# Kernel optimization log

Measured on AMD Instinct MI355X. Metric: run time of the kernel, lower is better.

Reference implementation:

```python
import jax, jax.numpy as jnp
import numpy as np

E = 8          # num_experts
K = 2          # num_experts_per_tok
NORM_TOPK = True
B, S, D, F = 2, 1024, 2048, 1024  # batch, seq, hidden, moe_intermediate


def _kaiming_uniform(key, shape):
    # moe_fused_kaiming_uniform_: bound = sqrt(3*5 / in_features), in_features = shape[-1]
    bound = float(np.sqrt(3.0 * 5.0 / shape[-1]))
    return jax.random.uniform(key, shape, jnp.float32, -bound, bound)


def setup_inputs() -> dict:
    key = jax.random.key(0)
    k0, k1, k2, k3, k4 = jax.random.split(key, 5)
    gate_bound = float(1.0 / np.sqrt(D))  # nn.Linear default init
    return {
        "hidden_states": jax.random.normal(k0, (B, S, D), jnp.float32),
        "gate_w": jax.random.uniform(k1, (E, D), jnp.float32, -gate_bound, gate_bound),
        "w_gate_proj": _kaiming_uniform(k2, (E, F, D)),
        "w_up_proj": _kaiming_uniform(k3, (E, F, D)),
        "w_down_proj": _kaiming_uniform(k4, (E, D, F)),
    }


def reference(hidden_states, gate_w, w_gate_proj, w_up_proj, w_down_proj):
    b, s, d = hidden_states.shape
    x = hidden_states.reshape(-1, d)                      # [T, D]
    T = x.shape[0]

    # Router: softmax in fp32, top-k, optional renorm
    router_logits = x @ gate_w.T                          # [T, E]
    probs = jax.nn.softmax(router_logits.astype(jnp.float32), axis=-1)
    routing_weights, selected = jax.lax.top_k(probs, K)   # [T, K], [T, K]
    if NORM_TOPK:
        routing_weights = routing_weights / routing_weights.sum(-1, keepdims=True)
    routing_weights = routing_weights.astype(x.dtype)

    # Dense combine weights: c[t, e] = sum_k rw[t,k] * (sel[t,k]==e)
    combine = jnp.zeros((T, E), x.dtype).at[jnp.arange(T)[:, None], selected].add(routing_weights)

    # Expert SwiGLU FFN (dense over experts; combine zeros out unrouted experts,
    # identical math to sorted grouped-GEMM dispatch in the original)
    g = jnp.einsum('td,efd->tef', x, w_gate_proj)         # [T, E, F]
    u = jnp.einsum('td,efd->tef', x, w_up_proj)           # [T, E, F]
    h = jax.nn.silu(g) * u                                # [T, E, F]
    out = jnp.einsum('tef,edf,te->td', h, w_down_proj, combine)  # [T, D]

    return out.reshape(b, s, d), router_logits
```

## Files before the change

kernel.cpp:

```cpp
#include <hip/hip_runtime.h>
#include <stdint.h>

#define T_TOK 2048
#define DIM   2048
#define FDIM  1024
#define NE    8
#define MAXTILES 40

typedef __attribute__((ext_vector_type(8))) short short8;
typedef __attribute__((ext_vector_type(4))) float f32x4;

__device__ __forceinline__ unsigned short f2b(float f) {
  union { float f; unsigned int i; } x; x.f = f;
  unsigned int r = x.i + 0x7fffu + ((x.i >> 16) & 1u);
  return (unsigned short)(r >> 16);
}

__device__ __forceinline__ void async16(void* lds, const void* g) {
  __builtin_amdgcn_global_load_lds(
      (const __attribute__((address_space(1))) void*)g,
      (__attribute__((address_space(3))) void*)lds, 16, 0, 0);
}

__global__ __launch_bounds__(256) void cvt_w_k(const float* __restrict__ src,
                                               unsigned short* __restrict__ dst)
{
  size_t i = ((size_t)blockIdx.x * 256 + threadIdx.x) * 8;
  float4 a = *(const float4*)(src + i);
  float4 b = *(const float4*)(src + i + 4);
  ushort4 o0, o1;
  o0.x = f2b(a.x); o0.y = f2b(a.y); o0.z = f2b(a.z); o0.w = f2b(a.w);
  o1.x = f2b(b.x); o1.y = f2b(b.y); o1.z = f2b(b.z); o1.w = f2b(b.w);
  *(ushort4*)(dst + i) = o0;
  *(ushort4*)(dst + i + 4) = o1;
}

__global__ __launch_bounds__(256) void router_k(
    const float* __restrict__ x, const float* __restrict__ gw,
    float* __restrict__ topkw, int* __restrict__ topke, int* __restrict__ counts,
    float* __restrict__ logits_out, unsigned short* __restrict__ xb)
{
  int wave = threadIdx.x >> 6, lane = threadIdx.x & 63;
  int t = blockIdx.x * 4 + wave;
  const float* xr = x + (size_t)t * DIM;
  unsigned short* xbr = xb + (size_t)t * DIM;
  float acc[NE];
#pragma unroll
  for (int e = 0; e < NE; e++) acc[e] = 0.f;
  for (int d = lane * 4; d < DIM; d += 256) {
    float4 xv = *(const float4*)(xr + d);
    ushort4 xo;
    xo.x = f2b(xv.x); xo.y = f2b(xv.y); xo.z = f2b(xv.z); xo.w = f2b(xv.w);
    *(ushort4*)(xbr + d) = xo;
#pragma unroll
    for (int e = 0; e < NE; e++) {
      float4 gv = *(const float4*)(gw + e * DIM + d);
      acc[e] += xv.x * gv.x + xv.y * gv.y + xv.z * gv.z + xv.w * gv.w;
    }
  }
#pragma unroll
  for (int off = 32; off > 0; off >>= 1) {
#pragma unroll
    for (int e = 0; e < NE; e++) acc[e] += __shfl_down(acc[e], off);
  }
  if (lane == 0) {
    float m = acc[0];
#pragma unroll
    for (int e = 1; e < NE; e++) m = fmaxf(m, acc[e]);
    float p[NE];
#pragma unroll
    for (int e = 0; e < NE; e++) p[e] = __expf(acc[e] - m);
    int e0 = 0;
#pragma unroll
    for (int e = 1; e < NE; e++) if (acc[e] > acc[e0]) e0 = e;
    int e1 = -1;
#pragma unroll
    for (int e = 0; e < NE; e++) if (e != e0 && (e1 < 0 || acc[e] > acc[e1])) e1 = e;
    float s = p[e0] + p[e1];
    topkw[t * 2] = p[e0] / s;
    topkw[t * 2 + 1] = p[e1] / s;
    topke[t * 2] = e0; topke[t * 2 + 1] = e1;
    atomicAdd(&counts[e0], 1);
    atomicAdd(&counts[e1], 1);
#pragma unroll
    for (int e = 0; e < NE; e++) logits_out[t * NE + e] = acc[e];
  }
}

__global__ void scan_k(const int* __restrict__ counts, int* __restrict__ offsets,
                       int* __restrict__ cursors, int4* __restrict__ tiles,
                       int* __restrict__ ntiles)
{
  if (threadIdx.x == 0 && blockIdx.x == 0) {
    int o = 0, nt = 0;
    for (int e = 0; e < NE; e++) {
      offsets[e] = o; cursors[e] = o;
      int c = counts[e];
      for (int r = 0; r < c; r += 128) {
        int rows = c - r < 128 ? c - r : 128;
        tiles[nt] = make_int4(e, o + r, rows, 0);
        nt++;
      }
      o += c;
    }
    offsets[NE] = o;
    *ntiles = nt;
  }
}

__global__ void scatter_k(const int* __restrict__ topke, int* __restrict__ cursors,
                          int* __restrict__ perm)
{
  int i = blockIdx.x * blockDim.x + threadIdx.x;
  int e = topke[i];
  int s = atomicAdd(&cursors[e], 1);
  perm[s] = i;
}


__global__ __launch_bounds__(256) void gemm1_bf_k(
    const unsigned short* __restrict__ xb,
    const unsigned short* __restrict__ wgb,
    const unsigned short* __restrict__ wub,
    const int* __restrict__ perm, const float* __restrict__ topkw,
    const int4* __restrict__ tiles, const int* __restrict__ ntiles,
    unsigned short* __restrict__ H)
{
  __shared__ short As[128 * 32];
  __shared__ short Bgs[64 * 32];
  __shared__ short Bus[64 * 32];
  __shared__ int rowtok[128];
  __shared__ float roww[128];

  if (blockIdx.x >= *ntiles) return;
  int4 tm = tiles[blockIdx.x];
  int e = tm.x, row0 = tm.y, nrows = tm.z;
  int tid = threadIdx.x;
  if (tid < 128) {
    int r = tid < nrows ? tid : (nrows - 1);
    int pid = perm[row0 + r];
    rowtok[tid] = pid >> 1;
    roww[tid] = topkw[pid];
  }
  __syncthreads();

  int f0 = blockIdx.y * 64;
  int crow = tid >> 2;
  int ccol = (tid & 3) * 8;
  const unsigned short* a0 = xb + (size_t)rowtok[crow] * DIM + ccol;
  const unsigned short* a1 = xb + (size_t)rowtok[crow + 64] * DIM + ccol;
  const unsigned short* bg = wgb + ((size_t)e * FDIM + f0 + crow) * DIM + ccol;
  const unsigned short* bu = wub + ((size_t)e * FDIM + f0 + crow) * DIM + ccol;
  short* as0 = As + tid * 8;
  short* as1 = As + (256 + tid) * 8;
  short* bgs = Bgs + tid * 8;
  short* bus = Bus + tid * 8;

  int wave = tid >> 6, lane = tid & 63;
  int wm = wave >> 1, wn = wave & 1;
  int lrow = lane & 15, quad = lane >> 4;

  f32x4 accg[4][2], accu[4][2];
#pragma unroll
  for (int i = 0; i < 4; i++)
#pragma unroll
    for (int j = 0; j < 2; j++) {
      accg[i][j] = (f32x4){0.f, 0.f, 0.f, 0.f};
      accu[i][j] = (f32x4){0.f, 0.f, 0.f, 0.f};
    }

  const short* arp = As + (wm * 64 + lrow) * 32 + quad * 8;
  const short* bgp = Bgs + (wn * 32 + lrow) * 32 + quad * 8;
  const short* bup = Bus + (wn * 32 + lrow) * 32 + quad * 8;

#pragma unroll 1
  for (int k0 = 0; k0 < DIM; k0 += 32) {
    async16(as0, a0 + k0);
    async16(as1, a1 + k0);
    async16(bgs, bg + k0);
    async16(bus, bu + k0);
    __syncthreads();
    short8 af[4], bgf[2], buf2[2];
#pragma unroll
    for (int i = 0; i < 4; i++) af[i] = *(const short8*)(arp + i * 16 * 32);
#pragma unroll
    for (int j = 0; j < 2; j++) {
      bgf[j]  = *(const short8*)(bgp + j * 16 * 32);
      buf2[j] = *(const short8*)(bup + j * 16 * 32);
    }
#pragma unroll
    for (int i = 0; i < 4; i++)
#pragma unroll
      for (int j = 0; j < 2; j++) {
        accg[i][j] = __builtin_amdgcn_mfma_f32_16x16x32_bf16(af[i], bgf[j], accg[i][j], 0, 0, 0);
        accu[i][j] = __builtin_amdgcn_mfma_f32_16x16x32_bf16(af[i], buf2[j], accu[i][j], 0, 0, 0);
      }
    __syncthreads();
  }

#pragma unroll
  for (int i = 0; i < 4; i++) {
#pragma unroll
    for (int reg = 0; reg < 4; reg++) {
      int r = wm * 64 + i * 16 + quad * 4 + reg;
      if (r < nrows) {
        float w = roww[r];
#pragma unroll
        for (int j = 0; j < 2; j++) {
          float g = accg[i][j][reg], u = accu[i][j][reg];
          float h = g * u * w / (1.f + __expf(-g));
          H[(size_t)(row0 + r) * FDIM + f0 + wn * 32 + j * 16 + lrow] = f2b(h);
        }
      }
    }
  }
}

__global__ __launch_bounds__(256) void gemm2_bf_k(
    const unsigned short* __restrict__ H,
    const unsigned short* __restrict__ wdb,
    const int* __restrict__ perm,
    const int4* __restrict__ tiles, const int* __restrict__ ntiles,
    float* __restrict__ out)
{
  __shared__ short Hs[128 * 32];
  __shared__ short Bs[128 * 32];
  __shared__ int rowtok[128];

  if (blockIdx.x >= *ntiles) return;
  int4 tm = tiles[blockIdx.x];
  int e = tm.x, row0 = tm.y, nrows = tm.z;
  int tid = threadIdx.x;
  if (tid < 128) {
    int r = tid < nrows ? tid : (nrows - 1);
    rowtok[tid] = perm[row0 + r] >> 1;
  }
  __syncthreads();

  int d0 = blockIdx.y * 128;
  int crow = tid >> 2, ccol = (tid & 3) * 8;
  const unsigned short* a0 = H + (size_t)(row0 + crow) * FDIM + ccol;
  const unsigned short* a1 = H + (size_t)(row0 + crow + 64) * FDIM + ccol;
  const unsigned short* b0 = wdb + ((size_t)e * DIM + d0 + crow) * FDIM + ccol;
  const unsigned short* b1 = b0 + (size_t)64 * FDIM;
  short* hs0 = Hs + tid * 8;
  short* hs1 = Hs + (256 + tid) * 8;
  short* bs0 = Bs + tid * 8;
  short* bs1 = Bs + (256 + tid) * 8;

  int wave = tid >> 6, lane = tid & 63;
  int wm = wave >> 1, wn = wave & 1;
  int lrow = lane & 15, quad = lane >> 4;

  f32x4 acc[4][4];
#pragma unroll
  for (int i = 0; i < 4; i++)
#pragma unroll
    for (int j = 0; j < 4; j++) acc[i][j] = (f32x4){0.f, 0.f, 0.f, 0.f};

  const short* arp = Hs + (wm * 64 + lrow) * 32 + quad * 8;
  const short* brp = Bs + (wn * 64 + lrow) * 32 + quad * 8;

#pragma unroll 1
  for (int k0 = 0; k0 < FDIM; k0 += 32) {
    async16(hs0, a0 + k0);
    async16(hs1, a1 + k0);
    async16(bs0, b0 + k0);
    async16(bs1, b1 + k0);
    __syncthreads();
    short8 af[4], bf[4];
#pragma unroll
    for (int i = 0; i < 4; i++) af[i] = *(const short8*)(arp + i * 16 * 32);
#pragma unroll
    for (int j = 0; j < 4; j++) bf[j] = *(const short8*)(brp + j * 16 * 32);
#pragma unroll
    for (int i = 0; i < 4; i++)
#pragma unroll
      for (int j = 0; j < 4; j++)
        acc[i][j] = __builtin_amdgcn_mfma_f32_16x16x32_bf16(af[i], bf[j], acc[i][j], 0, 0, 0);
    __syncthreads();
  }

#pragma unroll
  for (int i = 0; i < 4; i++) {
#pragma unroll
    for (int reg = 0; reg < 4; reg++) {
      int r = wm * 64 + i * 16 + quad * 4 + reg;
      if (r < nrows) {
        int t = rowtok[r];
#pragma unroll
        for (int j = 0; j < 4; j++) {
          atomicAdd(&out[(size_t)t * DIM + d0 + wn * 64 + j * 16 + lrow], acc[i][j][reg]);
        }
      }
    }
  }
}


__global__ __launch_bounds__(256) void gemm1_f32_k(
    const unsigned short* __restrict__ xb,
    const float* __restrict__ wg,
    const float* __restrict__ wu,
    const int* __restrict__ perm, const float* __restrict__ topkw,
    const int4* __restrict__ tiles, const int* __restrict__ ntiles,
    unsigned short* __restrict__ H)
{
  __shared__ short As[128 * 32];
  __shared__ short Bgs[64 * 32];
  __shared__ short Bus[64 * 32];
  __shared__ int rowtok[128];
  __shared__ float roww[128];

  if (blockIdx.x >= *ntiles) return;
  int4 tm = tiles[blockIdx.x];
  int e = tm.x, row0 = tm.y, nrows = tm.z;
  int tid = threadIdx.x;
  if (tid < 128) {
    int r = tid < nrows ? tid : (nrows - 1);
    int pid = perm[row0 + r];
    rowtok[tid] = pid >> 1;
    roww[tid] = topkw[pid];
  }
  __syncthreads();

  int f0 = blockIdx.y * 64;
  int crow = tid >> 2;
  int ccol = (tid & 3) * 8;
  const unsigned short* a0 = xb + (size_t)rowtok[crow] * DIM + ccol;
  const unsigned short* a1 = xb + (size_t)rowtok[crow + 64] * DIM + ccol;
  const float* bg32 = wg + ((size_t)e * FDIM + f0 + crow) * DIM + ccol;
  const float* bu32 = wu + ((size_t)e * FDIM + f0 + crow) * DIM + ccol;
  short* as0 = As + tid * 8;
  short* as1 = As + (256 + tid) * 8;

  int wave = tid >> 6, lane = tid & 63;
  int wm = wave >> 1, wn = wave & 1;
  int lrow = lane & 15, quad = lane >> 4;

  f32x4 accg[4][2], accu[4][2];
#pragma unroll
  for (int i = 0; i < 4; i++)
#pragma unroll
    for (int j = 0; j < 2; j++) {
      accg[i][j] = (f32x4){0.f, 0.f, 0.f, 0.f};
      accu[i][j] = (f32x4){0.f, 0.f, 0.f, 0.f};
    }

  const short* arp = As + (wm * 64 + lrow) * 32 + quad * 8;
  const short* bgp = Bgs + (wn * 32 + lrow) * 32 + quad * 8;
  const short* bup = Bus + (wn * 32 + lrow) * 32 + quad * 8;

#pragma unroll 1
  for (int k0 = 0; k0 < DIM; k0 += 32) {
    async16(as0, a0 + k0);
    async16(as1, a1 + k0);
    float4 g0 = *(const float4*)(bg32 + k0);
    float4 g1 = *(const float4*)(bg32 + k0 + 4);
    float4 u0 = *(const float4*)(bu32 + k0);
    float4 u1 = *(const float4*)(bu32 + k0 + 4);
    short8 gs, us;
    gs[0] = f2b(g0.x); gs[1] = f2b(g0.y); gs[2] = f2b(g0.z); gs[3] = f2b(g0.w);
    gs[4] = f2b(g1.x); gs[5] = f2b(g1.y); gs[6] = f2b(g1.z); gs[7] = f2b(g1.w);
    us[0] = f2b(u0.x); us[1] = f2b(u0.y); us[2] = f2b(u0.z); us[3] = f2b(u0.w);
    us[4] = f2b(u1.x); us[5] = f2b(u1.y); us[6] = f2b(u1.z); us[7] = f2b(u1.w);
    *(short8*)(Bgs + tid * 8) = gs;
    *(short8*)(Bus + tid * 8) = us;
    __syncthreads();
    short8 af[4], bgf[2], buf2[2];
#pragma unroll
    for (int i = 0; i < 4; i++) af[i] = *(const short8*)(arp + i * 16 * 32);
#pragma unroll
    for (int j = 0; j < 2; j++) {
      bgf[j]  = *(const short8*)(bgp + j * 16 * 32);
      buf2[j] = *(const short8*)(bup + j * 16 * 32);
    }
#pragma unroll
    for (int i = 0; i < 4; i++)
#pragma unroll
      for (int j = 0; j < 2; j++) {
        accg[i][j] = __builtin_amdgcn_mfma_f32_16x16x32_bf16(af[i], bgf[j], accg[i][j], 0, 0, 0);
        accu[i][j] = __builtin_amdgcn_mfma_f32_16x16x32_bf16(af[i], buf2[j], accu[i][j], 0, 0, 0);
      }
    __syncthreads();
  }

#pragma unroll
  for (int i = 0; i < 4; i++) {
#pragma unroll
    for (int reg = 0; reg < 4; reg++) {
      int r = wm * 64 + i * 16 + quad * 4 + reg;
      if (r < nrows) {
        float w = roww[r];
#pragma unroll
        for (int j = 0; j < 2; j++) {
          float g = accg[i][j][reg], u = accu[i][j][reg];
          float h = g * u * w / (1.f + __expf(-g));
          H[(size_t)(row0 + r) * FDIM + f0 + wn * 32 + j * 16 + lrow] = f2b(h);
        }
      }
    }
  }
}

__global__ __launch_bounds__(256) void gemm2_f32_k(
    const unsigned short* __restrict__ H,
    const float* __restrict__ wd,
    const int* __restrict__ perm,
    const int4* __restrict__ tiles, const int* __restrict__ ntiles,
    float* __restrict__ out)
{
  __shared__ short Hs[128 * 32];
  __shared__ short Bs[64 * 32];
  __shared__ int rowtok[128];

  if (blockIdx.x >= *ntiles) return;
  int4 tm = tiles[blockIdx.x];
  int e = tm.x, row0 = tm.y, nrows = tm.z;
  int tid = threadIdx.x;
  if (tid < 128) {
    int r = tid < nrows ? tid : (nrows - 1);
    rowtok[tid] = perm[row0 + r] >> 1;
  }
  __syncthreads();

  int d0 = blockIdx.y * 64;
  int crow = tid >> 2, ccol = (tid & 3) * 8;
  const unsigned short* a0 = H + (size_t)(row0 + crow) * FDIM + ccol;
  const unsigned short* a1 = H + (size_t)(row0 + crow + 64) * FDIM + ccol;
  const float* b32 = wd + ((size_t)e * DIM + d0 + crow) * FDIM + ccol;
  short* hs0 = Hs + tid * 8;
  short* hs1 = Hs + (256 + tid) * 8;

  int wave = tid >> 6, lane = tid & 63;
  int wm = wave >> 1, wn = wave & 1;
  int lrow = lane & 15, quad = lane >> 4;

  f32x4 acc[4][2];
#pragma unroll
  for (int i = 0; i < 4; i++)
#pragma unroll
    for (int j = 0; j < 2; j++) acc[i][j] = (f32x4){0.f, 0.f, 0.f, 0.f};

  const short* arp = Hs + (wm * 64 + lrow) * 32 + quad * 8;
  const short* brp = Bs + (wn * 32 + lrow) * 32 + quad * 8;

#pragma unroll 1
  for (int k0 = 0; k0 < FDIM; k0 += 32) {
    async16(hs0, a0 + k0);
    async16(hs1, a1 + k0);
    float4 b0 = *(const float4*)(b32 + k0);
    float4 b1 = *(const float4*)(b32 + k0 + 4);
    short8 bsv;
    bsv[0] = f2b(b0.x); bsv[1] = f2b(b0.y); bsv[2] = f2b(b0.z); bsv[3] = f2b(b0.w);
    bsv[4] = f2b(b1.x); bsv[5] = f2b(b1.y); bsv[6] = f2b(b1.z); bsv[7] = f2b(b1.w);
    *(short8*)(Bs + tid * 8) = bsv;
    __syncthreads();
    short8 af[4], bf[2];
#pragma unroll
    for (int i = 0; i < 4; i++) af[i] = *(const short8*)(arp + i * 16 * 32);
#pragma unroll
    for (int j = 0; j < 2; j++) bf[j] = *(const short8*)(brp + j * 16 * 32);
#pragma unroll
    for (int i = 0; i < 4; i++)
#pragma unroll
      for (int j = 0; j < 2; j++)
        acc[i][j] = __builtin_amdgcn_mfma_f32_16x16x32_bf16(af[i], bf[j], acc[i][j], 0, 0, 0);
    __syncthreads();
  }

#pragma unroll
  for (int i = 0; i < 4; i++) {
#pragma unroll
    for (int reg = 0; reg < 4; reg++) {
      int r = wm * 64 + i * 16 + quad * 4 + reg;
      if (r < nrows) {
        int t = rowtok[r];
#pragma unroll
        for (int j = 0; j < 2; j++) {
          atomicAdd(&out[(size_t)t * DIM + d0 + wn * 32 + j * 16 + lrow], acc[i][j][reg]);
        }
      }
    }
  }
}

extern "C" void kernel_launch(void* const* d_in, const int* in_sizes, int n_in,
                              void* d_out, int out_size, void* d_ws, size_t ws_size,
                              hipStream_t stream)
{
  const float* x  = (const float*)d_in[0];
  const float* gw = (const float*)d_in[1];
  const float* wg = (const float*)d_in[2];
  const float* wu = (const float*)d_in[3];
  const float* wd = (const float*)d_in[4];
  float* out = (float*)d_out;
  float* logits_out = out + (size_t)T_TOK * DIM;

  char* ws = (char*)d_ws;
  float* topkw   = (float*)(ws + 0);
  int*   topke   = (int*)(ws + 16384);
  int*   counts  = (int*)(ws + 32768);
  int*   offsets = (int*)(ws + 32768 + 64);
  int*   cursors = (int*)(ws + 32768 + 128);
  int*   ntiles  = (int*)(ws + 32768 + 192);
  int4*  tiles   = (int4*)(ws + 32768 + 256);
  int*   perm    = (int*)(ws + 32768 + 2048);
  unsigned short* xb  = (unsigned short*)(ws + (1u << 16));
  unsigned short* H   = (unsigned short*)(ws + (9u  << 20));
  unsigned short* wgb = (unsigned short*)(ws + (18u << 20));
  unsigned short* wub = (unsigned short*)(ws + (50u << 20));
  unsigned short* wdb = wgb;
  const size_t WS_NEED = (size_t)82u << 20;

  hipMemsetAsync(d_out, 0, (size_t)out_size * sizeof(float), stream);
  hipMemsetAsync(counts, 0, 64, stream);

  router_k<<<T_TOK / 4, 256, 0, stream>>>(x, gw, topkw, topke, counts, logits_out, xb);
  scan_k<<<1, 64, 0, stream>>>(counts, offsets, cursors, tiles, ntiles);
  scatter_k<<<(T_TOK * 2) / 256, 256, 0, stream>>>(topke, cursors, perm);

  if (ws_size >= WS_NEED) {
    const int nblk = (NE * FDIM * DIM) / 2048;
    cvt_w_k<<<nblk, 256, 0, stream>>>(wg, wgb);
    cvt_w_k<<<nblk, 256, 0, stream>>>(wu, wub);
    gemm1_bf_k<<<dim3(MAXTILES, FDIM / 64), 256, 0, stream>>>(xb, wgb, wub, perm, topkw, tiles, ntiles, H);
    cvt_w_k<<<nblk, 256, 0, stream>>>(wd, wdb);
    gemm2_bf_k<<<dim3(MAXTILES, DIM / 128), 256, 0, stream>>>(H, wdb, perm, tiles, ntiles, out);
  } else {
    gemm1_f32_k<<<dim3(MAXTILES, FDIM / 64), 256, 0, stream>>>(xb, wg, wu, perm, topkw, tiles, ntiles, H);
    gemm2_f32_k<<<dim3(MAXTILES, DIM / 64), 256, 0, stream>>>(H, wd, perm, tiles, ntiles, out);
  }
}
```

Baseline: 418.4 us.

## Double-buffer LDS tiles in both expert GEMM kernels to overlap loads with MFMA

Both grouped GEMM kernels now use two LDS buffers. Each iteration prefetches the next K-slice with async global-to-LDS loads right after the barrier, then runs MFMA on the current slice. This removes the second barrier per iteration and hides global load latency behind compute. The cost is twice the LDS per block, which may lower occupancy, and the code now relies on the barrier's implicit wait for outstanding async loads to keep the buffers correct.

Result: faster. 407.6 us (-2.6%).

```diff
diff --git a/kernel.cpp b/kernel.cpp
--- a/kernel.cpp
+++ b/kernel.cpp
@@ -126,9 +126,9 @@
     const int4* __restrict__ tiles, const int* __restrict__ ntiles,
     unsigned short* __restrict__ H)
 {
-  __shared__ short As[128 * 32];
-  __shared__ short Bgs[64 * 32];
-  __shared__ short Bus[64 * 32];
+  __shared__ short As[2][128 * 32];
+  __shared__ short Bgs[2][64 * 32];
+  __shared__ short Bus[2][64 * 32];
   __shared__ int rowtok[128];
   __shared__ float roww[128];
 
@@ -151,10 +151,6 @@
   const unsigned short* a1 = xb + (size_t)rowtok[crow + 64] * DIM + ccol;
   const unsigned short* bg = wgb + ((size_t)e * FDIM + f0 + crow) * DIM + ccol;
   const unsigned short* bu = wub + ((size_t)e * FDIM + f0 + crow) * DIM + ccol;
-  short* as0 = As + tid * 8;
-  short* as1 = As + (256 + tid) * 8;
-  short* bgs = Bgs + tid * 8;
-  short* bus = Bus + tid * 8;
 
   int wave = tid >> 6, lane = tid & 63;
   int wm = wave >> 1, wn = wave & 1;
@@ -169,17 +165,27 @@
       accu[i][j] = (f32x4){0.f, 0.f, 0.f, 0.f};
     }
 
-  const short* arp = As + (wm * 64 + lrow) * 32 + quad * 8;
-  const short* bgp = Bgs + (wn * 32 + lrow) * 32 + quad * 8;
-  const short* bup = Bus + (wn * 32 + lrow) * 32 + quad * 8;
+  const int aoff = (wm * 64 + lrow) * 32 + quad * 8;
+  const int boff = (wn * 32 + lrow) * 32 + quad * 8;
+
+#define STAGE1(b, k)                                 \
+  do {                                               \
+    async16(&As[b][tid * 8], a0 + (k));              \
+    async16(&As[b][(256 + tid) * 8], a1 + (k));      \
+    async16(&Bgs[b][tid * 8], bg + (k));             \
+    async16(&Bus[b][tid * 8], bu + (k));             \
+  } while (0)
+
+  STAGE1(0, 0);
 
 #pragma unroll 1
   for (int k0 = 0; k0 < DIM; k0 += 32) {
-    async16(as0, a0 + k0);
-    async16(as1, a1 + k0);
-    async16(bgs, bg + k0);
-    async16(bus, bu + k0);
+    int b = (k0 >> 5) & 1;
     __syncthreads();
+    if (k0 + 32 < DIM) STAGE1(b ^ 1, k0 + 32);
+    const short* arp = &As[0][0] + b * (128 * 32) + aoff;
+    const short* bgp = &Bgs[0][0] + b * (64 * 32) + boff;
+    const short* bup = &Bus[0][0] + b * (64 * 32) + boff;
     short8 af[4], bgf[2], buf2[2];
 #pragma unroll
     for (int i = 0; i < 4; i++) af[i] = *(const short8*)(arp + i * 16 * 32);
@@ -195,8 +201,8 @@
         accg[i][j] = __builtin_amdgcn_mfma_f32_16x16x32_bf16(af[i], bgf[j], accg[i][j], 0, 0, 0);
         accu[i][j] = __builtin_amdgcn_mfma_f32_16x16x32_bf16(af[i], buf2[j], accu[i][j], 0, 0, 0);
       }
-    __syncthreads();
-  }
+  }
+#undef STAGE1
 
 #pragma unroll
   for (int i = 0; i < 4; i++) {
@@ -223,8 +229,8 @@
     const int4* __restrict__ tiles, const int* __restrict__ ntiles,
     float* __restrict__ out)
 {
-  __shared__ short Hs[128 * 32];
-  __shared__ short Bs[128 * 32];
+  __shared__ short Hs[2][128 * 32];
+  __shared__ short Bs[2][128 * 32];
   __shared__ int rowtok[128];
 
   if (blockIdx.x >= *ntiles) return;
@@ -243,10 +249,6 @@
   const unsigned short* a1 = H + (size_t)(row0 + crow + 64) * FDIM + ccol;
   const unsigned short* b0 = wdb + ((size_t)e * DIM + d0 + crow) * FDIM + ccol;
   const unsigned short* b1 = b0 + (size_t)64 * FDIM;
-  short* hs0 = Hs + tid * 8;
-  short* hs1 = Hs + (256 + tid) * 8;
-  short* bs0 = Bs + tid * 8;
-  short* bs1 = Bs + (256 + tid) * 8;
 
   int wave = tid >> 6, lane = tid & 63;
   int wm = wave >> 1, wn = wave & 1;
@@ -258,16 +260,26 @@
 #pragma unroll
     for (int j = 0; j < 4; j++) acc[i][j] = (f32x4){0.f, 0.f, 0.f, 0.f};
 
-  const short* arp = Hs + (wm * 64 + lrow) * 32 + quad * 8;
-  const short* brp = Bs + (wn * 64 + lrow) * 32 + quad * 8;
+  const int aoff = (wm * 64 + lrow) * 32 + quad * 8;
+  const int boff = (wn * 64 + lrow) * 32 + quad * 8;
+
+#define STAGE2(b, k)                                 \
+  do {                                               \
+    async16(&Hs[b][tid * 8], a0 + (k));              \
+    async16(&Hs[b][(256 + tid) * 8], a1 + (k));      \
+    async16(&Bs[b][tid * 8], b0 + (k));              \
+    async16(&Bs[b][(256 + tid) * 8], b1 + (k));      \
+  } while (0)
+
+  STAGE2(0, 0);
 
 #pragma unroll 1
   for (int k0 = 0; k0 < FDIM; k0 += 32) {
-    async16(hs0, a0 + k0);
-    async16(hs1, a1 + k0);
-    async16(bs0, b0 + k0);
-    async16(bs1, b1 + k0);
+    int b = (k0 >> 5) & 1;
     __syncthreads();
+    if (k0 + 32 < FDIM) STAGE2(b ^ 1, k0 + 32);
+    const short* arp = &Hs[0][0] + b * (128 * 32) + aoff;
+    const short* brp = &Bs[0][0] + b * (128 * 32) + boff;
     short8 af[4], bf[4];
 #pragma unroll
     for (int i = 0; i < 4; i++) af[i] = *(const short8*)(arp + i * 16 * 32);
@@ -278,8 +290,8 @@
 #pragma unroll
       for (int j = 0; j < 4; j++)
         acc[i][j] = __builtin_amdgcn_mfma_f32_16x16x32_bf16(af[i], bf[j], acc[i][j], 0, 0, 0);
-    __syncthreads();
-  }
+  }
+#undef STAGE2
 
 #pragma unroll
   for (int i = 0; i < 4; i++) {
```
